# Performance work log

Hardware: AMD Instinct MI355X
Metric: run time of the kernel (lower is better)

Reference implementation:

```python
import jax, jax.numpy as jnp
import numpy as np

N_NODES = 100000
N_EDGES = 1600000
IN_CH, HID_CH, OUT_CH = 64, 64, 32
N_GRAPHS = 128


def setup_inputs() -> dict:
    key = jax.random.key(0)
    ks = jax.random.split(key, 12)
    x = jax.random.normal(ks[0], (N_NODES, IN_CH), dtype=jnp.float32)
    edge_index = jax.random.randint(ks[1], (2, N_EDGES), 0, N_NODES, dtype=jnp.int64)
    batch = jnp.sort(jax.random.randint(ks[2], (N_NODES,), 0, N_GRAPHS, dtype=jnp.int64))

    def glorot(k, fan_in, fan_out):
        s = jnp.sqrt(6.0 / (fan_in + fan_out))
        return jax.random.uniform(k, (fan_in, fan_out), jnp.float32, -s, s)

    return {
        "x": x,
        "edge_index": edge_index,
        "batch": batch,
        "W1": glorot(ks[3], IN_CH, HID_CH), "b1": jnp.zeros((HID_CH,), jnp.float32),
        "W2": glorot(ks[4], HID_CH, HID_CH), "b2": jnp.zeros((HID_CH,), jnp.float32),
        "W3": glorot(ks[5], HID_CH, HID_CH), "b3": jnp.zeros((HID_CH,), jnp.float32),
        "Wl": glorot(ks[6], HID_CH, OUT_CH), "bl": jnp.zeros((OUT_CH,), jnp.float32),
    }


def _gcn_conv(x, W, b, src, dst, n_nodes):
    # PyG GCNConv: linear transform, add self-loops, sym-normalize, scatter-add.
    h = x @ W  # [N, F]
    loops = jnp.arange(n_nodes, dtype=src.dtype)
    s = jnp.concatenate([src, loops])  # message sources j
    d = jnp.concatenate([dst, loops])  # message targets i
    ones = jnp.ones(s.shape[0], dtype=h.dtype)
    deg = jax.ops.segment_sum(ones, d, num_segments=n_nodes)  # in-degree + self-loop
    dinv = jnp.where(deg > 0, jax.lax.rsqrt(deg), 0.0)
    norm = dinv[s] * dinv[d]  # [E+N]
    msg = h[s] * norm[:, None]  # gather + scale
    out = jax.ops.segment_sum(msg, d, num_segments=n_nodes)  # scatter-add
    return out + b


def reference(x, edge_index, batch, W1, b1, W2, b2, W3, b3, Wl, bl):
    n = x.shape[0]
    src, dst = edge_index[0], edge_index[1]
    h = jax.nn.relu(_gcn_conv(x, W1, b1, src, dst, n))
    h = jax.nn.relu(_gcn_conv(h, W2, b2, src, dst, n))
    h = jax.nn.relu(_gcn_conv(h, W3, b3, src, dst, n))
    # global_mean_pool over graph ids
    sums = jax.ops.segment_sum(h, batch, num_segments=N_GRAPHS)
    cnts = jax.ops.segment_sum(jnp.ones((n,), h.dtype), batch, num_segments=N_GRAPHS)
    pooled = sums / jnp.maximum(cnts, 1.0)[:, None]  # [G, HID]
    return pooled @ Wl + bl  # [G, OUT]
```

## Files before the change

kernel.cpp:

```cpp
#include <hip/hip_runtime.h>
#include <hip/hip_fp16.h>


#define CH 64
#define OC 32

#define BINW 512
#define NBK  196
#define BIN_CAP 40
#define BCHUNK 2048
#define GCAP 10240

typedef unsigned int u32;
typedef _Float16 f16;
typedef __attribute__((ext_vector_type(8))) _Float16 f16x8;
typedef __attribute__((ext_vector_type(4))) float f32x4;

__device__ __forceinline__ float2 upk(u32 u) {
    __half2 h = *reinterpret_cast<__half2*>(&u);
    return __half22float2(h);
}
__device__ __forceinline__ u32 pk2(float x, float y) {
    __half2 h = __floats2half2_rn(x, y);
    return *reinterpret_cast<u32*>(&h);
}

__global__ __launch_bounds__(256) void k_bin(const int* __restrict__ src, const int* __restrict__ dst,
                                             u32* __restrict__ gbuf, int* __restrict__ gcur, int E) {
    __shared__ u32 lst[NBK][BIN_CAP];
    __shared__ int lcnt[NBK];
    __shared__ int lbase[NBK];
    int tid = threadIdx.x;
    for (int i = tid; i < NBK; i += 256) lcnt[i] = 0;
    __syncthreads();
    int beg = blockIdx.x * BCHUNK;
    int end = min(beg + BCHUNK, E);
    for (int e = beg + tid; e < end; e += 256) {
        int d = dst[e];
        u32 u = (u32)src[e] | ((u32)(d & (BINW - 1)) << 17);
        int b = d >> 9;
        int p = atomicAdd(&lcnt[b], 1);
        if (p < BIN_CAP) lst[b][p] = u;
        else {
            int gp = atomicAdd(&gcur[b], 1);
            if (gp < GCAP) gbuf[(size_t)b * GCAP + gp] = u;
        }
    }
    __syncthreads();
    for (int b = tid; b < NBK; b += 256) {
        int c = min(lcnt[b], BIN_CAP);
        lbase[b] = atomicAdd(&gcur[b], c);
        lcnt[b] = c;
    }
    __syncthreads();
    int wid = tid >> 6, lane = tid & 63;
    for (int b = wid; b < NBK; b += 4) {
        int c = lcnt[b], base = lbase[b];
        for (int i = lane; i < c; i += 64)
            gbuf[(size_t)b * GCAP + base + i] = lst[b][i];
    }
}

__global__ __launch_bounds__(512) void k_csr(const u32* __restrict__ gbuf, const int* __restrict__ gcur,
                                             int* __restrict__ rowptr, float* __restrict__ dinv,
                                             int* __restrict__ col, int N) {
    __shared__ int h[BINW];
    __shared__ int sc[BINW];
    __shared__ int bb[256];
    int b = blockIdx.x, tid = threadIdx.x;
    if (tid < 256) bb[tid] = (tid < NBK) ? min(gcur[tid], GCAP) : 0;
    __syncthreads();
    for (int o = 1; o < 256; o <<= 1) {
        int add = (tid < 256 && tid >= o) ? bb[tid - o] : 0;
        __syncthreads();
        if (tid < 256) bb[tid] += add;
        __syncthreads();
    }
    int my_base = (b == 0) ? 0 : bb[b - 1];
    if (b == 0 && tid == 0) rowptr[N] = bb[NBK - 1];
    h[tid] = 0;
    __syncthreads();
    int c = min(gcur[b], GCAP);
    const u32* p = gbuf + (size_t)b * GCAP;
    for (int i = tid; i < c; i += 512) atomicAdd(&h[p[i] >> 17], 1);
    __syncthreads();
    int cnt = h[tid];
    sc[tid] = cnt;
    __syncthreads();
    for (int o = 1; o < BINW; o <<= 1) {
        int add = (tid >= o) ? sc[tid - o] : 0;
        __syncthreads();
        sc[tid] += add;
        __syncthreads();
    }
    int ex = my_base + sc[tid] - cnt;
    int node = b * BINW + tid;
    if (node < N) {
        rowptr[node] = ex;
        dinv[node] = rsqrtf((float)(cnt + 1));
    }
    h[tid] = ex;
    __syncthreads();
    for (int i = tid; i < c; i += 512) {
        u32 u = p[i];
        int pos = atomicAdd(&h[u >> 17], 1);
        col[pos] = (int)(u & 0x1FFFF);
    }
}

__global__ __launch_bounds__(256) void k_bounds(const int* __restrict__ batch, int* __restrict__ gstart,
                                                int n, int ngraphs) {
    int i = blockIdx.x * 256 + threadIdx.x;
    if (i >= n) return;
    int b = batch[i];
    int prev = (i == 0) ? -1 : batch[i - 1];
    for (int g = prev + 1; g <= b; g++) gstart[g] = i;
    if (i == n - 1) for (int g = b + 1; g <= ngraphs; g++) gstart[g] = n;
}

__global__ __launch_bounds__(512) void k_wconv(const float* __restrict__ W1, const float* __restrict__ W2,
                                               const float* __restrict__ W3, f16* __restrict__ Wpk) {
    const float* Ws[3] = {W1, W2, W3};
    const float* W = Ws[blockIdx.x];
    int tid = threadIdx.x;
    int i = tid >> 6, l = tid & 63;
    int s = i & 1, t4 = i >> 1;
    int kbase = s * 32 + ((l >> 4) * 8);
    int cc = t4 * 16 + (l & 15);
    f16* dst = Wpk + (((size_t)blockIdx.x * 8 + i) * 64 + l) * 8;
#pragma unroll
    for (int j = 0; j < 8; j++) dst[j] = (f16)W[(kbase + j) * 64 + cc];
}

__global__ __launch_bounds__(256) void k_gmfma_h(const f16* __restrict__ in, const f16x8* __restrict__ Wpk,
                                                 const float* __restrict__ dinv, f16* __restrict__ out, int n_nodes) {
    int lane = threadIdx.x & 63;
    int wv = blockIdx.x * 4 + (threadIdx.x >> 6);
    int ntiles = (n_nodes + 15) >> 4;
    if (wv >= ntiles) return;
    f16x8 bf[8];
#pragma unroll
    for (int i = 0; i < 8; i++) bf[i] = Wpk[i * 64 + lane];
    int r0 = lane & 15;
    int kc = (lane >> 4) * 8;
    int n0 = wv * 16;
    int ar = min(n0 + r0, n_nodes - 1);
    const f16* arow = in + (size_t)ar * CH + kc;
    f16x8 a0 = *(const f16x8*)(arow);
    f16x8 a1 = *(const f16x8*)(arow + 32);
    f32x4 z = {0.f, 0.f, 0.f, 0.f};
    f32x4 acc0 = z, acc1 = z, acc2 = z, acc3 = z;
    acc0 = __builtin_amdgcn_mfma_f32_16x16x32_f16(a0, bf[0], acc0, 0, 0, 0);
    acc0 = __builtin_amdgcn_mfma_f32_16x16x32_f16(a1, bf[1], acc0, 0, 0, 0);
    acc1 = __builtin_amdgcn_mfma_f32_16x16x32_f16(a0, bf[2], acc1, 0, 0, 0);
    acc1 = __builtin_amdgcn_mfma_f32_16x16x32_f16(a1, bf[3], acc1, 0, 0, 0);
    acc2 = __builtin_amdgcn_mfma_f32_16x16x32_f16(a0, bf[4], acc2, 0, 0, 0);
    acc2 = __builtin_amdgcn_mfma_f32_16x16x32_f16(a1, bf[5], acc2, 0, 0, 0);
    acc3 = __builtin_amdgcn_mfma_f32_16x16x32_f16(a0, bf[6], acc3, 0, 0, 0);
    acc3 = __builtin_amdgcn_mfma_f32_16x16x32_f16(a1, bf[7], acc3, 0, 0, 0);
    int rb = n0 + (lane >> 4) * 4;
    float4 dv = *(const float4*)(dinv + rb);
    float dva[4] = {dv.x, dv.y, dv.z, dv.w};
#pragma unroll
    for (int r = 0; r < 4; r++) {
        int nn = rb + r;
        if (nn < n_nodes) {
            f16* orow = out + (size_t)nn * CH + r0;
            orow[0]  = (f16)(acc0[r] * dva[r]);
            orow[16] = (f16)(acc1[r] * dva[r]);
            orow[32] = (f16)(acc2[r] * dva[r]);
            orow[48] = (f16)(acc3[r] * dva[r]);
        }
    }
}

__global__ __launch_bounds__(256) void k_gmfma_x(const float* __restrict__ in, const f16x8* __restrict__ Wpk,
                                                 const float* __restrict__ dinv, f16* __restrict__ out, int n_nodes) {
    int lane = threadIdx.x & 63;
    int wv = blockIdx.x * 4 + (threadIdx.x >> 6);
    int ntiles = (n_nodes + 15) >> 4;
    if (wv >= ntiles) return;
    f16x8 bf[8];
#pragma unroll
    for (int i = 0; i < 8; i++) bf[i] = Wpk[i * 64 + lane];
    int r0 = lane & 15;
    int kc = (lane >> 4) * 8;
    int n0 = wv * 16;
    int ar = min(n0 + r0, n_nodes - 1);
    const float* arow = in + (size_t)ar * CH + kc;
    float4 p0 = *(const float4*)(arow);
    float4 p1 = *(const float4*)(arow + 4);
    float4 q0 = *(const float4*)(arow + 32);
    float4 q1 = *(const float4*)(arow + 36);
    float pa[8] = {p0.x, p0.y, p0.z, p0.w, p1.x, p1.y, p1.z, p1.w};
    float qa[8] = {q0.x, q0.y, q0.z, q0.w, q1.x, q1.y, q1.z, q1.w};
    f16x8 a0, a1;
#pragma unroll
    for (int j = 0; j < 8; j++) { a0[j] = (f16)pa[j]; a1[j] = (f16)qa[j]; }
    f32x4 z = {0.f, 0.f, 0.f, 0.f};
    f32x4 acc0 = z, acc1 = z, acc2 = z, acc3 = z;
    acc0 = __builtin_amdgcn_mfma_f32_16x16x32_f16(a0, bf[0], acc0, 0, 0, 0);
    acc0 = __builtin_amdgcn_mfma_f32_16x16x32_f16(a1, bf[1], acc0, 0, 0, 0);
    acc1 = __builtin_amdgcn_mfma_f32_16x16x32_f16(a0, bf[2], acc1, 0, 0, 0);
    acc1 = __builtin_amdgcn_mfma_f32_16x16x32_f16(a1, bf[3], acc1, 0, 0, 0);
    acc2 = __builtin_amdgcn_mfma_f32_16x16x32_f16(a0, bf[4], acc2, 0, 0, 0);
    acc2 = __builtin_amdgcn_mfma_f32_16x16x32_f16(a1, bf[5], acc2, 0, 0, 0);
    acc3 = __builtin_amdgcn_mfma_f32_16x16x32_f16(a0, bf[6], acc3, 0, 0, 0);
    acc3 = __builtin_amdgcn_mfma_f32_16x16x32_f16(a1, bf[7], acc3, 0, 0, 0);
    int rb = n0 + (lane >> 4) * 4;
    float4 dv = *(const float4*)(dinv + rb);
    float dva[4] = {dv.x, dv.y, dv.z, dv.w};
#pragma unroll
    for (int r = 0; r < 4; r++) {
        int nn = rb + r;
        if (nn < n_nodes) {
            f16* orow = out + (size_t)nn * CH + r0;
            orow[0]  = (f16)(acc0[r] * dva[r]);
            orow[16] = (f16)(acc1[r] * dva[r]);
            orow[32] = (f16)(acc2[r] * dva[r]);
            orow[48] = (f16)(acc3[r] * dva[r]);
        }
    }
}

__global__ __launch_bounds__(256) void k_agg2(const u32* __restrict__ g, const int* __restrict__ rowptr,
                                              const int* __restrict__ col, const float* __restrict__ dinv,
                                              const float* __restrict__ bias, u32* __restrict__ h, int n_nodes) {
    int c2 = threadIdx.x & 31;
    int node = (blockIdx.x * 256 + threadIdx.x) >> 5;
    if (node >= n_nodes) return;
    int beg = rowptr[node], end = rowptr[node + 1];
    int deg = end - beg;
    float2 sf = upk(g[(size_t)node * 32 + c2]);
    float a0 = sf.x, a1 = sf.y;
    int nb = min(deg, 32);
    int jv = (c2 < nb) ? col[beg + c2] : 0;
    int s = 0;
    for (; s + 15 < nb; s += 16) {
        u32 uu[16];
#pragma unroll
        for (int i = 0; i < 16; i++) {
            int j = __shfl(jv, s + i, 32);
            uu[i] = g[(size_t)j * 32 + c2];
        }
#pragma unroll
        for (int i = 0; i < 16; i++) {
            float2 f = upk(uu[i]);
            a0 += f.x; a1 += f.y;
        }
    }
    for (; s + 3 < nb; s += 4) {
        u32 uu[4];
#pragma unroll
        for (int i = 0; i < 4; i++) {
            int j = __shfl(jv, s + i, 32);
            uu[i] = g[(size_t)j * 32 + c2];
        }
#pragma unroll
        for (int i = 0; i < 4; i++) {
            float2 f = upk(uu[i]);
            a0 += f.x; a1 += f.y;
        }
    }
    for (; s < nb; s++) {
        int j = __shfl(jv, s, 32);
        float2 f = upk(g[(size_t)j * 32 + c2]);
        a0 += f.x; a1 += f.y;
    }
    for (int k = beg + 32; k < end; k++) {
        float2 f = upk(g[(size_t)col[k] * 32 + c2]);
        a0 += f.x; a1 += f.y;
    }
    float dn = dinv[node];
    float2 bb = *(const float2*)(bias + 2 * c2);
    float h0 = fmaxf(fmaf(dn, a0, bb.x), 0.f);
    float h1 = fmaxf(fmaf(dn, a1, bb.y), 0.f);
    h[(size_t)node * 32 + c2] = pk2(h0, h1);
}

__global__ __launch_bounds__(512) void k_pool_head(const u32* __restrict__ h, const int* __restrict__ gstart,
                                                   const float* __restrict__ Wl, const float* __restrict__ bl,
                                                   float* __restrict__ out) {
    __shared__ float part[16][CH];
    __shared__ float mean[CH];
    int gg = blockIdx.x;
    int hw = threadIdx.x >> 5;
    int c2 = threadIdx.x & 31;
    int beg = gstart[gg], end = gstart[gg + 1];
    float a0 = 0.f, a1 = 0.f;
    for (int n = beg + hw; n < end; n += 16) {
        float2 f = upk(h[(size_t)n * 32 + c2]);
        a0 += f.x; a1 += f.y;
    }
    part[hw][2 * c2] = a0; part[hw][2 * c2 + 1] = a1;
    __syncthreads();
    if (threadIdx.x < CH) {
        int c = threadIdx.x;
        float s = 0.f;
#pragma unroll
        for (int i = 0; i < 16; i++) s += part[i][c];
        float inv = 1.0f / fmaxf((float)(end - beg), 1.0f);
        mean[c] = s * inv;
    }
    __syncthreads();
    if (threadIdx.x < OC) {
        int o = threadIdx.x;
        float a = bl[o];
#pragma unroll
        for (int c = 0; c < CH; c++) a = fmaf(mean[c], Wl[c * OC + o], a);
        out[gg * OC + o] = a;
    }
}

extern "C" void kernel_launch(void* const* d_in, const int* in_sizes, int n_in,
                              void* d_out, int out_size, void* d_ws, size_t ws_size,
                              hipStream_t stream) {
    const float* x    = (const float*)d_in[0];
    const int*   edge = (const int*)d_in[1];
    const int*   batch= (const int*)d_in[2];
    const float* W1 = (const float*)d_in[3]; const float* b1 = (const float*)d_in[4];
    const float* W2 = (const float*)d_in[5]; const float* b2 = (const float*)d_in[6];
    const float* W3 = (const float*)d_in[7]; const float* b3 = (const float*)d_in[8];
    const float* Wl = (const float*)d_in[9]; const float* bl = (const float*)d_in[10];
    float* out = (float*)d_out;

    const int N  = in_sizes[2];
    const int E  = in_sizes[1] / 2;
    const int NG = out_size / OC;
    const int* src = edge;
    const int* dst = edge + E;

    char* p = (char*)d_ws;
    auto alloc = [&](size_t bytes) -> void* { void* r = p; p += (bytes + 255) & ~(size_t)255; return r; };
    int*   rowptr = (int*)alloc((size_t)(N + 1) * 4);
    int*   col    = (int*)alloc((size_t)E * 4);
    float* dinv   = (float*)alloc((size_t)N * 4);
    int*   gstart = (int*)alloc((size_t)(NG + 1) * 4);
    int*   gcur   = (int*)alloc((size_t)NBK * 4);
    u32*   gbuf   = (u32*)alloc((size_t)NBK * GCAP * 4);
    f16*   Wpk    = (f16*)alloc((size_t)3 * 8 * 64 * 8 * 2);
    u32*   Ga     = (u32*)alloc((size_t)N * CH * 2);
    u32*   Hb     = (u32*)alloc((size_t)N * CH * 2);

    hipMemsetAsync(gcur, 0, (size_t)NBK * 4, stream);

    int nbl2 = (N * 32 + 255) / 256;
    int binb = (E + BCHUNK - 1) / BCHUNK;
    int gemb = ((N + 15) / 16 + 3) / 4;

    k_bin<<<binb, 256, 0, stream>>>(src, dst, gbuf, gcur, E);
    k_csr<<<NBK, 512, 0, stream>>>(gbuf, gcur, rowptr, dinv, col, N);
    k_bounds<<<(N + 255) / 256, 256, 0, stream>>>(batch, gstart, N, NG);
    k_wconv<<<3, 512, 0, stream>>>(W1, W2, W3, Wpk);

    const f16x8* Wp = (const f16x8*)Wpk;
    k_gmfma_x<<<gemb, 256, 0, stream>>>(x, Wp, dinv, (f16*)Ga, N);
    k_agg2<<<nbl2, 256, 0, stream>>>(Ga, rowptr, col, dinv, b1, Hb, N);
    k_gmfma_h<<<gemb, 256, 0, stream>>>((const f16*)Hb, Wp + 8 * 64, dinv, (f16*)Ga, N);
    k_agg2<<<nbl2, 256, 0, stream>>>(Ga, rowptr, col, dinv, b2, Hb, N);
    k_gmfma_h<<<gemb, 256, 0, stream>>>((const f16*)Hb, Wp + 16 * 64, dinv, (f16*)Ga, N);
    k_agg2<<<nbl2, 256, 0, stream>>>(Ga, rowptr, col, dinv, b3, Hb, N);
    k_pool_head<<<NG, 512, 0, stream>>>(Hb, gstart, Wl, bl, out);
}
```

Before: 211.0 us.

## Fuse neighbor aggregation with next layer's MFMA GEMM via shared memory

```diff
diff --git a/kernel.cpp b/kernel.cpp
--- a/kernel.cpp
+++ b/kernel.cpp
@@ -130,48 +130,6 @@
     f16* dst = Wpk + (((size_t)blockIdx.x * 8 + i) * 64 + l) * 8;
 #pragma unroll
     for (int j = 0; j < 8; j++) dst[j] = (f16)W[(kbase + j) * 64 + cc];
-}
-
-__global__ __launch_bounds__(256) void k_gmfma_h(const f16* __restrict__ in, const f16x8* __restrict__ Wpk,
-                                                 const float* __restrict__ dinv, f16* __restrict__ out, int n_nodes) {
-    int lane = threadIdx.x & 63;
-    int wv = blockIdx.x * 4 + (threadIdx.x >> 6);
-    int ntiles = (n_nodes + 15) >> 4;
-    if (wv >= ntiles) return;
-    f16x8 bf[8];
-#pragma unroll
-    for (int i = 0; i < 8; i++) bf[i] = Wpk[i * 64 + lane];
-    int r0 = lane & 15;
-    int kc = (lane >> 4) * 8;
-    int n0 = wv * 16;
-    int ar = min(n0 + r0, n_nodes - 1);
-    const f16* arow = in + (size_t)ar * CH + kc;
-    f16x8 a0 = *(const f16x8*)(arow);
-    f16x8 a1 = *(const f16x8*)(arow + 32);
-    f32x4 z = {0.f, 0.f, 0.f, 0.f};
-    f32x4 acc0 = z, acc1 = z, acc2 = z, acc3 = z;
-    acc0 = __builtin_amdgcn_mfma_f32_16x16x32_f16(a0, bf[0], acc0, 0, 0, 0);
-    acc0 = __builtin_amdgcn_mfma_f32_16x16x32_f16(a1, bf[1], acc0, 0, 0, 0);
-    acc1 = __builtin_amdgcn_mfma_f32_16x16x32_f16(a0, bf[2], acc1, 0, 0, 0);
-    acc1 = __builtin_amdgcn_mfma_f32_16x16x32_f16(a1, bf[3], acc1, 0, 0, 0);
-    acc2 = __builtin_amdgcn_mfma_f32_16x16x32_f16(a0, bf[4], acc2, 0, 0, 0);
-    acc2 = __builtin_amdgcn_mfma_f32_16x16x32_f16(a1, bf[5], acc2, 0, 0, 0);
-    acc3 = __builtin_amdgcn_mfma_f32_16x16x32_f16(a0, bf[6], acc3, 0, 0, 0);
-    acc3 = __builtin_amdgcn_mfma_f32_16x16x32_f16(a1, bf[7], acc3, 0, 0, 0);
-    int rb = n0 + (lane >> 4) * 4;
-    float4 dv = *(const float4*)(dinv + rb);
-    float dva[4] = {dv.x, dv.y, dv.z, dv.w};
-#pragma unroll
-    for (int r = 0; r < 4; r++) {
-        int nn = rb + r;
-        if (nn < n_nodes) {
-            f16* orow = out + (size_t)nn * CH + r0;
-            orow[0]  = (f16)(acc0[r] * dva[r]);
-            orow[16] = (f16)(acc1[r] * dva[r]);
-            orow[32] = (f16)(acc2[r] * dva[r]);
-            orow[48] = (f16)(acc3[r] * dva[r]);
-        }
-    }
 }
 
 __global__ __launch_bounds__(256) void k_gmfma_x(const float* __restrict__ in, const f16x8* __restrict__ Wpk,
@@ -219,6 +177,103 @@
             orow[16] = (f16)(acc1[r] * dva[r]);
             orow[32] = (f16)(acc2[r] * dva[r]);
             orow[48] = (f16)(acc3[r] * dva[r]);
+        }
+    }
+}
+
+__global__ __launch_bounds__(512) void k_aggemm(const u32* __restrict__ g, const int* __restrict__ rowptr,
+                                                const int* __restrict__ col, const float* __restrict__ dinv,
+                                                const float* __restrict__ bias, const f16x8* __restrict__ Wpk,
+                                                f16* __restrict__ gout, int n_nodes) {
+    __shared__ u32 hrow[64][36];
+    int tid = threadIdx.x;
+    int c2 = tid & 31;
+    int hw = tid >> 5;
+    int base = blockIdx.x * 64;
+#pragma unroll
+    for (int i = 0; i < 4; i++) {
+        int nl = hw * 4 + i;
+        int node = base + nl;
+        if (node < n_nodes) {
+            int beg = rowptr[node], end = rowptr[node + 1];
+            int deg = end - beg;
+            float2 sf = upk(g[(size_t)node * 32 + c2]);
+            float a0 = sf.x, a1 = sf.y;
+            int nb = min(deg, 32);
+            int jv = (c2 < nb) ? col[beg + c2] : 0;
+            int s = 0;
+            for (; s + 15 < nb; s += 16) {
+                u32 uu[16];
+#pragma unroll
+                for (int q = 0; q < 16; q++) {
+                    int j = __shfl(jv, s + q, 32);
+                    uu[q] = g[(size_t)j * 32 + c2];
+                }
+#pragma unroll
+                for (int q = 0; q < 16; q++) {
+                    float2 f = upk(uu[q]);
+                    a0 += f.x; a1 += f.y;
+                }
+            }
+            for (; s + 3 < nb; s += 4) {
+                u32 uu[4];
+#pragma unroll
+                for (int q = 0; q < 4; q++) {
+                    int j = __shfl(jv, s + q, 32);
+                    uu[q] = g[(size_t)j * 32 + c2];
+                }
+#pragma unroll
+                for (int q = 0; q < 4; q++) {
+                    float2 f = upk(uu[q]);
+                    a0 += f.x; a1 += f.y;
+                }
+            }
+            for (; s < nb; s++) {
+                int j = __shfl(jv, s, 32);
+                float2 f = upk(g[(size_t)j * 32 + c2]);
+                a0 += f.x; a1 += f.y;
+            }
+            for (int k = beg + 32; k < end; k++) {
+                float2 f = upk(g[(size_t)col[k] * 32 + c2]);
+                a0 += f.x; a1 += f.y;
+            }
+            float dn = dinv[node];
+            float2 bb = *(const float2*)(bias + 2 * c2);
+            hrow[nl][c2] = pk2(fmaxf(fmaf(dn, a0, bb.x), 0.f),
+                               fmaxf(fmaf(dn, a1, bb.y), 0.f));
+        } else {
+            hrow[nl][c2] = 0;
+        }
+    }
+    __syncthreads();
+    int wid = tid >> 6;
+    int lane = tid & 63;
+    int tile = wid >> 1;
+    int colh = wid & 1;
+    f16x8 bfa = Wpk[(colh * 4 + 0) * 64 + lane];
+    f16x8 bfb = Wpk[(colh * 4 + 1) * 64 + lane];
+    f16x8 bfc = Wpk[(colh * 4 + 2) * 64 + lane];
+    f16x8 bfd = Wpk[(colh * 4 + 3) * 64 + lane];
+    int r0 = lane & 15;
+    int k4 = (lane >> 4) * 4;
+    const u32* hr = &hrow[tile * 16 + r0][0];
+    f16x8 a0 = *(const f16x8*)(hr + k4);
+    f16x8 a1 = *(const f16x8*)(hr + 16 + k4);
+    f32x4 z = {0.f, 0.f, 0.f, 0.f};
+    f32x4 acc0 = z, acc1 = z;
+    acc0 = __builtin_amdgcn_mfma_f32_16x16x32_f16(a0, bfa, acc0, 0, 0, 0);
+    acc0 = __builtin_amdgcn_mfma_f32_16x16x32_f16(a1, bfb, acc0, 0, 0, 0);
+    acc1 = __builtin_amdgcn_mfma_f32_16x16x32_f16(a0, bfc, acc1, 0, 0, 0);
+    acc1 = __builtin_amdgcn_mfma_f32_16x16x32_f16(a1, bfd, acc1, 0, 0, 0);
+    int rb = base + tile * 16 + (lane >> 4) * 4;
+#pragma unroll
+    for (int r = 0; r < 4; r++) {
+        int nn = rb + r;
+        if (nn < n_nodes) {
+            float dn = dinv[nn];
+            f16* orow = gout + (size_t)nn * CH + colh * 32 + r0;
+            orow[0]  = (f16)(acc0[r] * dn);
+            orow[16] = (f16)(acc1[r] * dn);
         }
     }
 }
@@ -347,6 +402,7 @@
     int nbl2 = (N * 32 + 255) / 256;
     int binb = (E + BCHUNK - 1) / BCHUNK;
     int gemb = ((N + 15) / 16 + 3) / 4;
+    int fusb = (N + 63) / 64;
 
     k_bin<<<binb, 256, 0, stream>>>(src, dst, gbuf, gcur, E);
     k_csr<<<NBK, 512, 0, stream>>>(gbuf, gcur, rowptr, dinv, col, N);
@@ -355,10 +411,10 @@
 
     const f16x8* Wp = (const f16x8*)Wpk;
     k_gmfma_x<<<gemb, 256, 0, stream>>>(x, Wp, dinv, (f16*)Ga, N);
-    k_agg2<<<nbl2, 256, 0, stream>>>(Ga, rowptr, col, dinv, b1, Hb, N);
-    k_gmfma_h<<<gemb, 256, 0, stream>>>((const f16*)Hb, Wp + 8 * 64, dinv, (f16*)Ga, N);
-    k_agg2<<<nbl2, 256, 0, stream>>>(Ga, rowptr, col, dinv, b2, Hb, N);
-    k_gmfma_h<<<gemb, 256, 0, stream>>>((const f16*)Hb, Wp + 16 * 64, dinv, (f16*)Ga, N);
+    k_aggemm<<<fusb, 512, 0, stream>>>(Ga, rowptr, col, dinv, b1, Wp + 8 * 64,
+                                       (f16*)Hb, N);
+    k_aggemm<<<fusb, 512, 0, stream>>>(Hb, rowptr, col, dinv, b2, Wp + 16 * 64,
+                                       (f16*)Ga, N);
     k_agg2<<<nbl2, 256, 0, stream>>>(Ga, rowptr, col, dinv, b3, Hb, N);
     k_pool_head<<<NG, 512, 0, stream>>>(Hb, gstart, Wl, bl, out);
 }
```

After: 220.2 us. +4.4%, slower.
